# Optimization experiments

Hardware: AMD Instinct MI355X
Metric: run time of the kernel (lower is better)

## Reference

```python
import jax, jax.numpy as jnp
import numpy as np

B, T, D_IN = 64, 512, 512
D_HID, D_OUT = 1024, 512
NUM_DAYS = 24
EPS = 1e-5


def setup_inputs() -> dict:
    key = jax.random.key(0)
    ks = jax.random.split(key, 8)
    x = jax.random.normal(ks[0], (B, T, D_IN), dtype=jnp.float32)
    day_indices = jax.random.randint(ks[1], (B,), 0, NUM_DAYS)
    s1 = 1.0 / np.sqrt(D_IN)
    s2 = 1.0 / np.sqrt(D_HID)
    W1 = jax.random.uniform(ks[2], (NUM_DAYS, D_IN, D_HID), jnp.float32, -s1, s1)
    b1 = jax.random.uniform(ks[3], (NUM_DAYS, D_HID), jnp.float32, -s1, s1)
    W2 = jax.random.uniform(ks[4], (NUM_DAYS, D_HID, D_OUT), jnp.float32, -s2, s2)
    b2 = jax.random.uniform(ks[5], (NUM_DAYS, D_OUT), jnp.float32, -s2, s2)
    gamma = jnp.ones((NUM_DAYS, D_OUT), jnp.float32)
    beta = jnp.zeros((NUM_DAYS, D_OUT), jnp.float32)
    return {"x": x, "day_indices": day_indices, "W1": W1, "b1": b1,
            "W2": W2, "b2": b2, "gamma": gamma, "beta": beta}


def reference(x, day_indices, W1, b1, W2, b2, gamma, beta):
    # Gather each sample's day-specific adapter params, then one batched pass.
    # Equivalent to the per-day mask/gather/scatter loop in the torch module.
    # Dropout is identity (eval mode).
    W1d = W1[day_indices]                      # [B, D_in, D_hid]
    b1d = b1[day_indices][:, None, :]          # [B, 1, D_hid]
    W2d = W2[day_indices]                      # [B, D_hid, D_out]
    b2d = b2[day_indices][:, None, :]          # [B, 1, D_out]
    h = jax.nn.relu(jnp.einsum('btd,bdh->bth', x, W1d) + b1d)
    y = jnp.einsum('bth,bho->bto', h, W2d) + b2d
    # per-day LayerNorm over last dim
    mean = jnp.mean(y, axis=-1, keepdims=True)
    var = jnp.var(y, axis=-1, keepdims=True)
    y_hat = (y - mean) * jax.lax.rsqrt(var + EPS)
    g = gamma[day_indices][:, None, :]
    bt = beta[day_indices][:, None, :]
    return y_hat * g + bt
```

## Files before the change

### kernel.cpp

```cpp
#include <hip/hip_runtime.h>

#define B_    64
#define T_    512
#define DIN   512
#define DHID  1024
#define DOUT  512
#define NDAYS 24

typedef unsigned short u16;
typedef __bf16 bf16x8 __attribute__((ext_vector_type(8)));
typedef u16    u16x8  __attribute__((ext_vector_type(8)));
typedef float  f32x4  __attribute__((ext_vector_type(4)));

static __device__ __forceinline__ u16 f2bf(float f) {
    union { float f; unsigned u; } v; v.f = f;
    unsigned r = v.u + 0x7FFFu + ((v.u >> 16) & 1u);
    return (u16)(r >> 16);
}

static __device__ __forceinline__ void gload_lds16(const void* g, void* l) {
    __builtin_amdgcn_global_load_lds(
        (const __attribute__((address_space(1))) void*)g,
        (__attribute__((address_space(3))) void*)l, 16, 0, 0);
}

__global__ __launch_bounds__(256)
void transpose_w(const float* __restrict__ W, u16* __restrict__ WT, int R, int C) {
    __shared__ float t[32][33];
    const int d  = blockIdx.z;
    const int r0 = blockIdx.y * 32, c0 = blockIdx.x * 32;
    const int tx = threadIdx.x, ty = threadIdx.y;
    const float* Wd = W + (size_t)d * R * C;
    u16* WTd = WT + (size_t)d * R * C;
#pragma unroll
    for (int i = 0; i < 4; ++i)
        t[ty + i * 8][tx] = Wd[(size_t)(r0 + ty + i * 8) * C + c0 + tx];
    __syncthreads();
#pragma unroll
    for (int i = 0; i < 4; ++i)
        WTd[(size_t)(c0 + ty + i * 8) * R + r0 + tx] = f2bf(t[tx][ty + i * 8]);
}

__global__ __launch_bounds__(256)
void cvt_bf16(const float* __restrict__ in, u16* __restrict__ outp, int n8) {
    int i = blockIdx.x * 256 + threadIdx.x;
    const int stride = gridDim.x * 256;
    for (; i < n8; i += stride) {
        float4 a = ((const float4*)in)[i * 2];
        float4 b = ((const float4*)in)[i * 2 + 1];
        u16x8 p;
        p[0] = f2bf(a.x); p[1] = f2bf(a.y); p[2] = f2bf(a.z); p[3] = f2bf(a.w);
        p[4] = f2bf(b.x); p[5] = f2bf(b.y); p[6] = f2bf(b.z); p[7] = f2bf(b.w);
        ((u16x8*)outp)[i] = p;
    }
}

template<int MT, int NT, int KT, bool RELU, bool OUT_BF16>
__global__ __launch_bounds__(512, 1)
void gemm8(const u16* __restrict__ Aall,
           const u16* __restrict__ BT,
           const float* __restrict__ bias,
           const int* __restrict__ didx,
           void* __restrict__ Call)
{
    constexpr int GX = MT / 256;
    constexpr int GY = NT / 256;
    constexpr int NWG = GX * GY * B_;
    constexpr int NT_K = KT / 64;
    static_assert(NT_K >= 2 && (NWG % 8) == 0, "geometry");

    constexpr int Q = NWG / 8;
    const int hw = blockIdx.x;
    const int l  = (hw & 7) * Q + (hw >> 3);
    const int bx = l % GX;
    const int by = (l / GX) % GY;
    const int bz = l / (GX * GY);

    const int day = didx[bz];
    const int m0 = bx * 256, n0 = by * 256;
    const int tid = threadIdx.x;
    const int wv = tid >> 6, ln = tid & 63;
    const int wm = wv >> 2, wn = wv & 3;

    __shared__ __align__(16) u16 sA[2][256 * 64];
    __shared__ __align__(16) u16 sB[2][256 * 64];

    const u16* Ab = Aall + (size_t)bz * MT * KT + (size_t)m0 * KT;
    const u16* Bt = BT + (size_t)day * NT * KT + (size_t)n0 * KT;

    auto stageA = [&](int buf, int t, int h) {
#pragma unroll
        for (int c = 0; c < 2; ++c) {
            const int rl = h * 128 + wv * 16 + c * 8 + (ln >> 3);
            const int cd = (ln & 7) ^ (rl & 7);
            gload_lds16(Ab + (size_t)rl * KT + t * 64 + cd * 8,
                        (char*)&sA[buf][(h * 128 + wv * 16 + c * 8) * 64]);
        }
    };
    auto stageB = [&](int buf, int t, int h) {
#pragma unroll
        for (int c = 0; c < 2; ++c) {
            const int rl = h * 128 + wv * 16 + c * 8 + (ln >> 3);
            const int cd = (ln & 7) ^ (rl & 7);
            gload_lds16(Bt + (size_t)rl * KT + t * 64 + cd * 8,
                        (char*)&sB[buf][(h * 128 + wv * 16 + c * 8) * 64]);
        }
    };

    f32x4 acc[8][4];
#pragma unroll
    for (int i = 0; i < 8; ++i)
#pragma unroll
        for (int j = 0; j < 4; ++j)
            acc[i][j] = (f32x4){0.f, 0.f, 0.f, 0.f};

    stageA(0, 0, 0); stageB(0, 0, 0); stageA(0, 0, 1); stageB(0, 0, 1);
    stageA(1, 1, 0); stageB(1, 1, 0);
    asm volatile("s_waitcnt vmcnt(4)" ::: "memory");
    __builtin_amdgcn_s_barrier();

    for (int t = 0; t < NT_K; ++t) {
        const int buf = t & 1;
        const u16* sAb = sA[buf];
        const u16* sBb = sB[buf];
        bf16x8 av[2][4], bv[2][2];

#pragma unroll
        for (int p = 0; p < 4; ++p) {
            const int mq = p >> 1, nq = p & 1;
            if (p == 0 || p == 2) {
#pragma unroll
                for (int ks = 0; ks < 2; ++ks)
#pragma unroll
                    for (int mi = 0; mi < 4; ++mi) {
                        const int r = mq * 128 + wm * 64 + mi * 16 + (ln & 15);
                        const int slot = (ks * 4 + (ln >> 4)) ^ (r & 7);
                        av[ks][mi] = *(const bf16x8*)&sAb[r * 64 + slot * 8];
                    }
            }
#pragma unroll
            for (int ks = 0; ks < 2; ++ks)
#pragma unroll
                for (int ni = 0; ni < 2; ++ni) {
                    const int r = nq * 128 + wn * 32 + ni * 16 + (ln & 15);
                    const int slot = (ks * 4 + (ln >> 4)) ^ (r & 7);
                    bv[ks][ni] = *(const bf16x8*)&sBb[r * 64 + slot * 8];
                }
            if (p == 0)      { if (t + 1 < NT_K) stageA(buf ^ 1, t + 1, 1); }
            else if (p == 1) { if (t + 1 < NT_K) stageB(buf ^ 1, t + 1, 1); }
            else if (p == 2) { if (t + 2 < NT_K) stageA(buf, t + 2, 0); }
            else             { if (t + 2 < NT_K) stageB(buf, t + 2, 0); }

            __builtin_amdgcn_s_barrier();
            asm volatile("s_waitcnt lgkmcnt(0)" ::: "memory");
            __builtin_amdgcn_sched_barrier(0);
            __builtin_amdgcn_s_setprio(1);
#pragma unroll
            for (int ks = 0; ks < 2; ++ks)
#pragma unroll
                for (int mi = 0; mi < 4; ++mi)
#pragma unroll
                    for (int ni = 0; ni < 2; ++ni)
                        acc[mq * 4 + mi][nq * 2 + ni] =
                            __builtin_amdgcn_mfma_f32_16x16x32_bf16(
                                av[ks][mi], bv[ks][ni],
                                acc[mq * 4 + mi][nq * 2 + ni], 0, 0, 0);
            __builtin_amdgcn_s_setprio(0);
            if (p == 3) {
                if (t + 2 < NT_K) asm volatile("s_waitcnt vmcnt(4)" ::: "memory");
                else              asm volatile("s_waitcnt vmcnt(0)" ::: "memory");
            }
            __builtin_amdgcn_s_barrier();
        }
    }

    const float* bs = bias + (size_t)day * NT + n0;
#pragma unroll
    for (int nq = 0; nq < 2; ++nq)
#pragma unroll
        for (int ni = 0; ni < 2; ++ni) {
            const int col = nq * 128 + wn * 32 + ni * 16 + (ln & 15);
            const float bval = bs[col];
#pragma unroll
            for (int mq = 0; mq < 2; ++mq)
#pragma unroll
                for (int mi = 0; mi < 4; ++mi)
#pragma unroll
                    for (int i = 0; i < 4; ++i) {
                        const int row = mq * 128 + wm * 64 + mi * 16 + (ln >> 4) * 4 + i;
                        float v = acc[mq * 4 + mi][nq * 2 + ni][i] + bval;
                        if (RELU) v = fmaxf(v, 0.f);
                        const size_t off = (size_t)bz * MT * NT + (size_t)(m0 + row) * NT + (n0 + col);
                        if (OUT_BF16) ((u16*)Call)[off] = f2bf(v);
                        else          ((float*)Call)[off] = v;
                    }
        }
}

__global__ __launch_bounds__(256)
void ln_kernel(float* __restrict__ y, const int* __restrict__ didx,
               const float* __restrict__ gamma, const float* __restrict__ beta)
{
    const int row = blockIdx.x * 4 + (threadIdx.x >> 6);
    const int ln  = threadIdx.x & 63;
    const int b   = row >> 9;
    const int day = didx[b];
    float* p = y + (size_t)row * DOUT;

    float4 v0 = ((const float4*)p)[ln];
    float4 v1 = ((const float4*)p)[64 + ln];
    float s = v0.x + v0.y + v0.z + v0.w + v1.x + v1.y + v1.z + v1.w;
    float q = v0.x * v0.x + v0.y * v0.y + v0.z * v0.z + v0.w * v0.w
            + v1.x * v1.x + v1.y * v1.y + v1.z * v1.z + v1.w * v1.w;
#pragma unroll
    for (int o = 32; o; o >>= 1) { s += __shfl_xor(s, o); q += __shfl_xor(q, o); }
    const float mean = s * (1.f / 512.f);
    const float var  = q * (1.f / 512.f) - mean * mean;
    const float rstd = rsqrtf(var + 1e-5f);

    const float4* g  = (const float4*)(gamma + (size_t)day * DOUT);
    const float4* bt = (const float4*)(beta  + (size_t)day * DOUT);
    float4 g0 = g[ln], g1 = g[64 + ln], bb0 = bt[ln], bb1 = bt[64 + ln];
    float4 o0, o1;
    o0.x = (v0.x - mean) * rstd * g0.x + bb0.x;
    o0.y = (v0.y - mean) * rstd * g0.y + bb0.y;
    o0.z = (v0.z - mean) * rstd * g0.z + bb0.z;
    o0.w = (v0.w - mean) * rstd * g0.w + bb0.w;
    o1.x = (v1.x - mean) * rstd * g1.x + bb1.x;
    o1.y = (v1.y - mean) * rstd * g1.y + bb1.y;
    o1.z = (v1.z - mean) * rstd * g1.z + bb1.z;
    o1.w = (v1.w - mean) * rstd * g1.w + bb1.w;
    ((float4*)p)[ln] = o0;
    ((float4*)p)[64 + ln] = o1;
}

extern "C" void kernel_launch(void* const* d_in, const int* in_sizes, int n_in,
                              void* d_out, int out_size, void* d_ws, size_t ws_size,
                              hipStream_t stream)
{
    const float* x     = (const float*)d_in[0];
    const int*   didx  = (const int*)d_in[1];
    const float* W1    = (const float*)d_in[2];
    const float* b1    = (const float*)d_in[3];
    const float* W2    = (const float*)d_in[4];
    const float* b2    = (const float*)d_in[5];
    const float* gamma = (const float*)d_in[6];
    const float* beta  = (const float*)d_in[7];
    float* out = (float*)d_out;

    char* ws = (char*)d_ws;
    u16* W1T = (u16*)ws;
    u16* h   = (u16*)(ws + 25165824);
    u16* xb  = (u16*)(ws + 92274688);
    u16* W2T = xb;

    transpose_w<<<dim3(DHID / 32, DIN / 32, NDAYS), dim3(32, 8), 0, stream>>>(W1, W1T, DIN, DHID);
    cvt_bf16<<<2048, 256, 0, stream>>>(x, xb, B_ * T_ * DIN / 8);

    gemm8<T_, DHID, DIN, true, true>
        <<<dim3(2 * 4 * B_), 512, 0, stream>>>(xb, W1T, b1, didx, h);

    transpose_w<<<dim3(DOUT / 32, DHID / 32, NDAYS), dim3(32, 8), 0, stream>>>(W2, W2T, DHID, DOUT);

    gemm8<T_, DOUT, DHID, false, false>
        <<<dim3(2 * 2 * B_), 512, 0, stream>>>(h, W2T, b2, didx, out);

    ln_kernel<<<(B_ * T_) / 4, 256, 0, stream>>>(out, didx, gamma, beta);
}
```

Before: 166.6 us.

## Fuse second GEMM with LayerNorm using full-row 128x512 tiles

Replaces the second gemm8 launch and the separate LayerNorm kernel with one kernel in which each workgroup computes a 128-row by full 512-column output tile. Row statistics are reduced with shuffles and shared memory, and the normalized result is written once. This removes the fp32 write and re-read of the 64 MB output and one kernel launch. In exchange the tile is larger, giving 256 workgroups with launch bounds of one block per SM, which lowers occupancy and raises register pressure. It also uses a new staged pipeline with a larger B tile in LDS.

```diff
diff --git a/kernel.cpp b/kernel.cpp
--- a/kernel.cpp
+++ b/kernel.cpp
@@ -197,41 +197,188 @@
         }
 }
 
-__global__ __launch_bounds__(256)
-void ln_kernel(float* __restrict__ y, const int* __restrict__ didx,
-               const float* __restrict__ gamma, const float* __restrict__ beta)
+__global__ __launch_bounds__(512, 1)
+void gemm2_ln(const u16* __restrict__ Aall,
+              const u16* __restrict__ BT,
+              const float* __restrict__ bias,
+              const int* __restrict__ didx,
+              const float* __restrict__ gamma,
+              const float* __restrict__ beta,
+              float* __restrict__ out)
 {
-    const int row = blockIdx.x * 4 + (threadIdx.x >> 6);
-    const int ln  = threadIdx.x & 63;
-    const int b   = row >> 9;
-    const int day = didx[b];
-    float* p = y + (size_t)row * DOUT;
-
-    float4 v0 = ((const float4*)p)[ln];
-    float4 v1 = ((const float4*)p)[64 + ln];
-    float s = v0.x + v0.y + v0.z + v0.w + v1.x + v1.y + v1.z + v1.w;
-    float q = v0.x * v0.x + v0.y * v0.y + v0.z * v0.z + v0.w * v0.w
-            + v1.x * v1.x + v1.y * v1.y + v1.z * v1.z + v1.w * v1.w;
-#pragma unroll
-    for (int o = 32; o; o >>= 1) { s += __shfl_xor(s, o); q += __shfl_xor(q, o); }
-    const float mean = s * (1.f / 512.f);
-    const float var  = q * (1.f / 512.f) - mean * mean;
-    const float rstd = rsqrtf(var + 1e-5f);
-
-    const float4* g  = (const float4*)(gamma + (size_t)day * DOUT);
-    const float4* bt = (const float4*)(beta  + (size_t)day * DOUT);
-    float4 g0 = g[ln], g1 = g[64 + ln], bb0 = bt[ln], bb1 = bt[64 + ln];
-    float4 o0, o1;
-    o0.x = (v0.x - mean) * rstd * g0.x + bb0.x;
-    o0.y = (v0.y - mean) * rstd * g0.y + bb0.y;
-    o0.z = (v0.z - mean) * rstd * g0.z + bb0.z;
-    o0.w = (v0.w - mean) * rstd * g0.w + bb0.w;
-    o1.x = (v1.x - mean) * rstd * g1.x + bb1.x;
-    o1.y = (v1.y - mean) * rstd * g1.y + bb1.y;
-    o1.z = (v1.z - mean) * rstd * g1.z + bb1.z;
-    o1.w = (v1.w - mean) * rstd * g1.w + bb1.w;
-    ((float4*)p)[ln] = o0;
-    ((float4*)p)[64 + ln] = o1;
+    constexpr int BM = 128, BK = 64;
+    constexpr int KT = DHID;
+    constexpr int NT_K = KT / BK;
+    constexpr int GX = T_ / BM;
+    constexpr int NWG = GX * B_;
+
+    constexpr int Q = NWG / 8;
+    const int hw = blockIdx.x;
+    const int l  = (hw & 7) * Q + (hw >> 3);
+    const int bx = l % GX;
+    const int bz = l / GX;
+
+    const int day = didx[bz];
+    const int m0 = bx * BM;
+    const int tid = threadIdx.x;
+    const int wv = tid >> 6, ln = tid & 63;
+    const int wm = wv >> 2, wn = wv & 3;
+
+    __shared__ __align__(16) u16 sA[2][BM * BK];
+    __shared__ __align__(16) u16 sB[2][DOUT * BK];
+
+    const u16* Ab = Aall + (size_t)bz * T_ * KT + (size_t)m0 * KT;
+    const u16* Bt = BT + (size_t)day * DOUT * KT;
+
+    auto stageA = [&](int buf, int t) {
+#pragma unroll
+        for (int c = 0; c < 2; ++c) {
+            const int rl = wv * 16 + c * 8 + (ln >> 3);
+            const int cd = (ln & 7) ^ (rl & 7);
+            gload_lds16(Ab + (size_t)rl * KT + t * BK + cd * 8,
+                        (char*)&sA[buf][(wv * 16 + c * 8) * BK]);
+        }
+    };
+    auto stageBh = [&](int buf, int t, int h) {
+#pragma unroll
+        for (int c = 0; c < 4; ++c) {
+            const int rl = h * 256 + wv * 32 + c * 8 + (ln >> 3);
+            const int cd = (ln & 7) ^ (rl & 7);
+            gload_lds16(Bt + (size_t)rl * KT + t * BK + cd * 8,
+                        (char*)&sB[buf][(h * 256 + wv * 32 + c * 8) * BK]);
+        }
+    };
+
+    f32x4 acc[4][8];
+#pragma unroll
+    for (int i = 0; i < 4; ++i)
+#pragma unroll
+        for (int j = 0; j < 8; ++j)
+            acc[i][j] = (f32x4){0.f, 0.f, 0.f, 0.f};
+
+    stageA(0, 0); stageBh(0, 0, 0); stageBh(0, 0, 1);
+    stageA(1, 1); stageBh(1, 1, 0);
+    asm volatile("s_waitcnt vmcnt(6)" ::: "memory");
+    __builtin_amdgcn_s_barrier();
+
+    for (int t = 0; t < NT_K; ++t) {
+        const int buf = t & 1;
+        const u16* sAb = sA[buf];
+        const u16* sBb = sB[buf];
+        bf16x8 av[2][4], bv[2][2];
+
+#pragma unroll
+        for (int p = 0; p < 4; ++p) {
+            if (p == 0) {
+#pragma unroll
+                for (int ks = 0; ks < 2; ++ks)
+#pragma unroll
+                    for (int mi = 0; mi < 4; ++mi) {
+                        const int r = wm * 64 + mi * 16 + (ln & 15);
+                        const int slot = (ks * 4 + (ln >> 4)) ^ (r & 7);
+                        av[ks][mi] = *(const bf16x8*)&sAb[r * BK + slot * 8];
+                    }
+            }
+#pragma unroll
+            for (int ks = 0; ks < 2; ++ks)
+#pragma unroll
+                for (int ni = 0; ni < 2; ++ni) {
+                    const int r = p * 128 + wn * 32 + ni * 16 + (ln & 15);
+                    const int slot = (ks * 4 + (ln >> 4)) ^ (r & 7);
+                    bv[ks][ni] = *(const bf16x8*)&sBb[r * BK + slot * 8];
+                }
+            if (p == 0)      { if (t + 1 < NT_K) stageBh(buf ^ 1, t + 1, 1); }
+            else if (p == 1) { if (t + 2 < NT_K) stageA(buf, t + 2); }
+            else if (p == 2) { if (t + 2 < NT_K) stageBh(buf, t + 2, 0); }
+
+            __builtin_amdgcn_s_barrier();
+            asm volatile("s_waitcnt lgkmcnt(0)" ::: "memory");
+            __builtin_amdgcn_sched_barrier(0);
+            __builtin_amdgcn_s_setprio(1);
+#pragma unroll
+            for (int ks = 0; ks < 2; ++ks)
+#pragma unroll
+                for (int mi = 0; mi < 4; ++mi)
+#pragma unroll
+                    for (int ni = 0; ni < 2; ++ni)
+                        acc[mi][p * 2 + ni] =
+                            __builtin_amdgcn_mfma_f32_16x16x32_bf16(
+                                av[ks][mi], bv[ks][ni], acc[mi][p * 2 + ni], 0, 0, 0);
+            __builtin_amdgcn_s_setprio(0);
+            if (p == 3) {
+                if (t + 2 < NT_K) asm volatile("s_waitcnt vmcnt(6)" ::: "memory");
+                else              asm volatile("s_waitcnt vmcnt(0)" ::: "memory");
+            }
+            __builtin_amdgcn_s_barrier();
+        }
+    }
+
+    const float* bs = bias + (size_t)day * DOUT;
+    const float* gs = gamma + (size_t)day * DOUT;
+    const float* es = beta + (size_t)day * DOUT;
+    float bval[8], gval[8], eval_[8];
+#pragma unroll
+    for (int f = 0; f < 8; ++f) {
+        const int col = (f >> 1) * 128 + wn * 32 + (f & 1) * 16 + (ln & 15);
+        bval[f] = bs[col]; gval[f] = gs[col]; eval_[f] = es[col];
+    }
+
+    float ps[4][4], pq[4][4];
+#pragma unroll
+    for (int mi = 0; mi < 4; ++mi)
+#pragma unroll
+        for (int i = 0; i < 4; ++i) {
+            float s = 0.f, q = 0.f;
+#pragma unroll
+            for (int f = 0; f < 8; ++f) {
+                const float v = acc[mi][f][i] + bval[f];
+                s += v; q += v * v;
+            }
+            ps[mi][i] = s; pq[mi][i] = q;
+        }
+#pragma unroll
+    for (int o = 1; o < 16; o <<= 1)
+#pragma unroll
+        for (int mi = 0; mi < 4; ++mi)
+#pragma unroll
+            for (int i = 0; i < 4; ++i) {
+                ps[mi][i] += __shfl_xor(ps[mi][i], o);
+                pq[mi][i] += __shfl_xor(pq[mi][i], o);
+            }
+
+    float* sLN = (float*)&sA[0][0];
+    if ((ln & 15) == 0) {
+#pragma unroll
+        for (int mi = 0; mi < 4; ++mi)
+#pragma unroll
+            for (int i = 0; i < 4; ++i) {
+                const int rloc = wm * 64 + mi * 16 + (ln >> 4) * 4 + i;
+                sLN[rloc * 8 + wn * 2 + 0] = ps[mi][i];
+                sLN[rloc * 8 + wn * 2 + 1] = pq[mi][i];
+            }
+    }
+    __syncthreads();
+
+    float* op = out + (size_t)bz * T_ * DOUT + (size_t)m0 * DOUT;
+#pragma unroll
+    for (int mi = 0; mi < 4; ++mi)
+#pragma unroll
+        for (int i = 0; i < 4; ++i) {
+            const int rloc = wm * 64 + mi * 16 + (ln >> 4) * 4 + i;
+            const float s = sLN[rloc * 8 + 0] + sLN[rloc * 8 + 2]
+                          + sLN[rloc * 8 + 4] + sLN[rloc * 8 + 6];
+            const float q = sLN[rloc * 8 + 1] + sLN[rloc * 8 + 3]
+                          + sLN[rloc * 8 + 5] + sLN[rloc * 8 + 7];
+            const float mean = s * (1.f / 512.f);
+            const float var  = q * (1.f / 512.f) - mean * mean;
+            const float rstd = rsqrtf(var + 1e-5f);
+#pragma unroll
+            for (int f = 0; f < 8; ++f) {
+                const int col = (f >> 1) * 128 + wn * 32 + (f & 1) * 16 + (ln & 15);
+                const float v = acc[mi][f][i] + bval[f];
+                op[(size_t)rloc * DOUT + col] = (v - mean) * rstd * gval[f] + eval_[f];
+            }
+        }
 }
 
 extern "C" void kernel_launch(void* const* d_in, const int* in_sizes, int n_in,
@@ -262,8 +409,5 @@
 
     transpose_w<<<dim3(DOUT / 32, DHID / 32, NDAYS), dim3(32, 8), 0, stream>>>(W2, W2T, DHID, DOUT);
 
-    gemm8<T_, DOUT, DHID, false, false>
-        <<<dim3(2 * 2 * B_), 512, 0, stream>>>(h, W2T, b2, didx, out);
-
-    ln_kernel<<<(B_ * T_) / 4, 256, 0, stream>>>(out, didx, gamma, beta);
-}
+    gemm2_ln<<<dim3(4 * B_), 512, 0, stream>>>(h, W2T, b2, didx, gamma, beta, out);
+}
```

Result: slower. 190.8 us (+14.5%).
